# Kernel optimization log

Measured on AMD Instinct MI355X. Metric: run time of the kernel, lower is better.

Reference implementation:

```python
import jax, jax.numpy as jnp
import numpy as np

BS, SL, FD = 8192, 49, 11
D_MODEL, DM2, HEAD = 128, 64, 8
NH, NHID, NLAYER = DM2 // HEAD, 4, 2
ABF = 1.0
XY_IDX = np.array([0, 1, 2, 3, 4, 5, 6, 7, 10])  # x feats + y feat (batch-normed cols)
DEC_IN = D_MODEL + 10  # d_model + len(x_dims + spa_dims)


def tanhshrink(x):
    return x - jnp.tanh(x)


def rope_angles(spa):
    # spa: [bs, sl, 2] -> per-token block angles [bs, sl, 4]
    # block order matches torch.block_diag(Rx(t0), Ry(t0), Rx(t1), Ry(t1))
    thetas = 10000.0 ** ((2.0 - 2.0 * jnp.arange(2, dtype=spa.dtype)) / 8.0)  # d=8, n_thetas=2
    ax = spa[..., 0:1] * thetas  # [bs, sl, 2]
    ay = spa[..., 1:2] * thetas
    return jnp.stack([ax[..., 0], ay[..., 0], ax[..., 1], ay[..., 1]], axis=-1)


def apply_rope(v, ang):
    # v: [bs, nh, s, 8]; ang: [bs, s, 4]. Applies the 8x8 block-diagonal
    # rotation directly on 2-d sub-pairs (same math as R @ v, no 8x8 matmats).
    c = jnp.cos(ang)[:, None]  # [bs, 1, s, 4]
    s = jnp.sin(ang)[:, None]
    v2 = v.reshape(*v.shape[:-1], 4, 2)
    r = jnp.stack([c * v2[..., 0] - s * v2[..., 1],
                   s * v2[..., 0] + c * v2[..., 1]], axis=-1)
    return r.reshape(v.shape)


def heads(x):  # [bs, s, dm2] -> [bs, nh, s, hd]
    b, s, _ = x.shape
    return x.reshape(b, s, NH, HEAD).transpose(0, 2, 1, 3)


def merge(x):  # [bs, nh, s, hd] -> [bs, s, dm2]
    b, h, s, d = x.shape
    return x.transpose(0, 2, 1, 3).reshape(b, s, h * d)


def mlp2(x, w1, b1, w2, b2):
    return tanhshrink(x @ w1 + b1) @ w2 + b2


def forward_impl(input_tensor, dists, bn_gamma, bn_beta,
                 xe_w1, xe_b1, xe_w2, xe_b2, ye_w1, ye_b1, ye_w2, ye_b2,
                 learnable_y, hidden_tokens, Wq, Wk, Wv, Wo, Wq2, Wk2, Wv2, Wo2,
                 dec_w0, dec_b0, dec_w1, dec_b1, dec_w2, dec_b2):
    bs = input_tensor.shape[0]
    # --- NanBatchNorm over x+y feature columns (no NaNs in clean inputs) ---
    xy = input_tensor[:, :, XY_IDX]
    mu = jnp.mean(xy, axis=(0, 1), keepdims=True)
    var = jnp.var(xy, axis=(0, 1), keepdims=True)
    xy = (xy - mu) / jnp.sqrt(var + 1e-5) * bn_gamma + bn_beta
    input_tensor = input_tensor.at[:, :, XY_IDX].set(xy)

    # --- target at last seq position: drop its dist, keep context dists ---
    dists_ctx = dists[:, :-1]                       # [bs, sl-1]
    central_x = input_tensor[:, -1:, :-1]           # [bs, 1, 10] (x + spa feats)

    # --- 2D RoPE angles from spatial coords ---
    ang = rope_angles(input_tensor[:, :, 8:10])     # [bs, sl, 4]

    # --- FCN encoders (two streams a=x, b=y) ---
    x_embed = mlp2(input_tensor[:, :, :8], xe_w1, xe_b1, xe_w2, xe_b2)      # [bs, sl, 64]
    y_embed = mlp2(input_tensor[:, :-1, 10:11], ye_w1, ye_b1, ye_w2, ye_b2)  # [bs, sl-1, 64]
    y_embed = jnp.concatenate([y_embed, jnp.broadcast_to(learnable_y, (bs, 1, DM2))], axis=1)

    ctx = (x_embed[:, :-1], y_embed[:, :-1])
    qry = (x_embed[:, -1:], y_embed[:, -1:])
    ang_ctx, ang_q = ang[:, :-1], ang[:, -1:]
    bias = (-ABF * dists_ctx)[:, None, None, :]     # [bs, 1, 1, sl-1]
    scale = 1.0 / jnp.sqrt(jnp.asarray(HEAD, input_tensor.dtype))

    outs, attn_ws = [], []
    for s in range(2):
        H = jnp.broadcast_to(hidden_tokens, (bs, NHID, DM2))
        for l in range(NLAYER):
            q = heads(H @ Wq[l, s])
            k = apply_rope(heads(ctx[s] @ Wk[l, s]), ang_ctx)
            v = heads(ctx[s] @ Wv[l, s])
            sc = jnp.einsum('bhqd,bhkd->bhqk', q, k) * scale + bias
            a = jax.nn.softmax(sc, axis=-1)
            H = H + merge(jnp.einsum('bhqk,bhkd->bhqd', a, v)) @ Wo[l, s]
        # query cross-attends the inducing tokens
        q = apply_rope(heads(qry[s] @ Wq2[s]), ang_q)
        k = heads(H @ Wk2[s])
        v = heads(H @ Wv2[s])
        sc = jnp.einsum('bhqd,bhkd->bhqk', q, k) * scale
        a = jax.nn.softmax(sc, axis=-1)
        outs.append(merge(jnp.einsum('bhqk,bhkd->bhqd', a, v)) @ Wo2[s])  # [bs, 1, 64]
        attn_ws.append(a)

    encoding = jnp.concatenate(outs, axis=-1)               # [bs, 1, 128]
    encoding = jnp.concatenate([encoding, central_x], axis=-1)  # [bs, 1, 138]
    h = tanhshrink(encoding @ dec_w0 + dec_b0)
    h = tanhshrink(h @ dec_w1 + dec_b1)
    pred = h @ dec_w2 + dec_b2                              # [bs, 1, 1]
    return pred


def setup_inputs() -> dict:
    key = jax.random.key(0)
    ks = jax.random.split(key, 32)
    g = lambda i, shape: 0.05 * jax.random.normal(ks[i], shape, dtype=jnp.float32)
    inp = {
        'input_tensor': jax.random.normal(ks[0], (BS, SL, FD), dtype=jnp.float32),
        'dists': jax.random.uniform(ks[1], (BS, SL), dtype=jnp.float32),
        'target_position': jnp.zeros((3, BS), dtype=jnp.int32),
        'bn_gamma': jnp.ones((9,), jnp.float32),
        'bn_beta': jnp.zeros((9,), jnp.float32),
        'xe_w1': g(2, (8, DM2)), 'xe_b1': jnp.zeros((DM2,), jnp.float32),
        'xe_w2': g(3, (DM2, DM2)), 'xe_b2': jnp.zeros((DM2,), jnp.float32),
        'ye_w1': g(4, (1, DM2)), 'ye_b1': jnp.zeros((DM2,), jnp.float32),
        'ye_w2': g(5, (DM2, DM2)), 'ye_b2': jnp.zeros((DM2,), jnp.float32),
        'learnable_y': g(6, (1, 1, DM2)),
        'hidden_tokens': g(7, (NHID, DM2)),
        'Wq': g(8, (NLAYER, 2, DM2, DM2)), 'Wk': g(9, (NLAYER, 2, DM2, DM2)),
        'Wv': g(10, (NLAYER, 2, DM2, DM2)), 'Wo': g(11, (NLAYER, 2, DM2, DM2)),
        'Wq2': g(12, (2, DM2, DM2)), 'Wk2': g(13, (2, DM2, DM2)),
        'Wv2': g(14, (2, DM2, DM2)), 'Wo2': g(15, (2, DM2, DM2)),
        'dec_w0': g(16, (DEC_IN, 512)), 'dec_b0': jnp.zeros((512,), jnp.float32),
        'dec_w1': g(17, (512, 256)), 'dec_b1': jnp.zeros((256,), jnp.float32),
        'dec_w2': g(18, (256, 1)), 'dec_b2': jnp.zeros((1,), jnp.float32),
    }
    return inp


def reference(input_tensor, dists, target_position, bn_gamma, bn_beta,
              xe_w1, xe_b1, xe_w2, xe_b2, ye_w1, ye_b1, ye_w2, ye_b2,
              learnable_y, hidden_tokens, Wq, Wk, Wv, Wo, Wq2, Wk2, Wv2, Wo2,
              dec_w0, dec_b0, dec_w1, dec_b1, dec_w2, dec_b2):
    # target_position is an index constant (query is the last token by construction)
    return forward_impl(input_tensor, dists, bn_gamma, bn_beta,
                        xe_w1, xe_b1, xe_w2, xe_b2, ye_w1, ye_b1, ye_w2, ye_b2,
                        learnable_y, hidden_tokens, Wq, Wk, Wv, Wo, Wq2, Wk2, Wv2, Wo2,
                        dec_w0, dec_b0, dec_w1, dec_b1, dec_w2, dec_b2)
```

## Files before the change

kernel.cpp:

```cpp
#include <hip/hip_runtime.h>
#include <math.h>

#define BS 8192
#define SL 49
#define FDIM 11
#define ROWS (BS*SL)

__device__ __forceinline__ float tanhshrink_f(float x) {
  float e = __expf(2.f * x);
  return (x - 1.f) + __fdividef(2.f, e + 1.f);
}

__global__ __launch_bounds__(256) void k_stats(const float* __restrict__ inp,
                                               double* __restrict__ gsum) {
  const int nblk = gridDim.x;
  const int per = (ROWS + nblk - 1) / nblk;
  const int r0 = blockIdx.x * per;
  int r1 = r0 + per; if (r1 > ROWS) r1 = ROWS;
  float s[9], q[9];
#pragma unroll
  for (int j = 0; j < 9; ++j) { s[j] = 0.f; q[j] = 0.f; }
  for (int r = r0 + threadIdx.x; r < r1; r += 256) {
    const float* row = inp + r * FDIM;
#pragma unroll
    for (int j = 0; j < 9; ++j) {
      float v = row[j < 8 ? j : 10];
      s[j] += v; q[j] += v * v;
    }
  }
#pragma unroll
  for (int j = 0; j < 9; ++j) {
    for (int off = 32; off; off >>= 1) {
      s[j] += __shfl_down(s[j], off);
      q[j] += __shfl_down(q[j], off);
    }
  }
  __shared__ float red[4][18];
  const int wid = threadIdx.x >> 6;
  const int lane = threadIdx.x & 63;
  if (lane == 0) {
#pragma unroll
    for (int j = 0; j < 9; ++j) { red[wid][j] = s[j]; red[wid][9 + j] = q[j]; }
  }
  __syncthreads();
  if (threadIdx.x < 18) {
    float t = red[0][threadIdx.x] + red[1][threadIdx.x] +
              red[2][threadIdx.x] + red[3][threadIdx.x];
    atomicAdd(&gsum[threadIdx.x], (double)t);
  }
}

__global__ __launch_bounds__(256) void k_finalize(const double* __restrict__ gsum,
                           const float* __restrict__ gamma,
                           const float* __restrict__ beta,
                           const float* __restrict__ hidden,
                           const float* __restrict__ Wq,
                           float* __restrict__ bnp,
                           float* __restrict__ q0g) {
  int tid = threadIdx.x;
  if (tid < 9) {
    const double N = (double)ROWS;
    double mean = gsum[tid] / N;
    double msq  = gsum[9 + tid] / N;
    float var = (float)(msq - mean * mean);
    float sc = gamma[tid] / sqrtf(var + 1e-5f);
    bnp[tid] = sc;
    bnp[9 + tid] = beta[tid] - (float)mean * sc;
  }
  int s = tid >> 7, i2 = (tid >> 6) & 1, c = tid & 63;
  const float* W = Wq + (s << 12);
#pragma unroll
  for (int ii = 0; ii < 2; ++ii) {
    int i = i2 + 2 * ii;
    float a = 0.f;
    for (int k = 0; k < 64; ++k) a += hidden[i * 64 + k] * W[k * 64 + c];
    q0g[s * 256 + i * 64 + c] = a;
  }
}

__global__ __launch_bounds__(256, 4) void k_mega(
    const float* __restrict__ inp, const float* __restrict__ dists,
    const float* __restrict__ bnp, const float* __restrict__ q0g,
    const float* __restrict__ xe_w1, const float* __restrict__ xe_b1,
    const float* __restrict__ xe_w2, const float* __restrict__ xe_b2,
    const float* __restrict__ ye_w1, const float* __restrict__ ye_b1,
    const float* __restrict__ ye_w2, const float* __restrict__ ye_b2,
    const float* __restrict__ learnable_y, const float* __restrict__ hidden_tokens,
    const float* __restrict__ Wq, const float* __restrict__ Wk,
    const float* __restrict__ Wv, const float* __restrict__ Wo,
    const float* __restrict__ Wq2, const float* __restrict__ Wk2,
    const float* __restrict__ Wv2, const float* __restrict__ Wo2,
    float* __restrict__ enc)
{
  __shared__ float raw[49][12];
  __shared__ float cs8[49][8];
  __shared__ float emb[49][64];
  __shared__ float KB[49][68];
  __shared__ float scb[32][52];
  __shared__ float Hs[4][64];
  __shared__ float qb[4][64];
  __shared__ float db[48];
  __shared__ float bnl[18];
  __shared__ float q2[64];
  __shared__ float o1[64];
  __shared__ float a2[32];

  const int tid  = threadIdx.x;
  const int lane = tid & 63;
  const int grp  = tid >> 6;
  const int b    = blockIdx.x >> 1;
  const int s    = blockIdx.x & 1;
  const float scale = 0.35355339059327373f;

  for (int i = tid; i < 49 * FDIM; i += 256) raw[i / FDIM][i % FDIM] = inp[b * (49*FDIM) + i];
  if (tid < 18) bnl[tid] = bnp[tid];
  if (tid >= 64 && tid < 112) db[tid - 64] = dists[b * 49 + (tid - 64)];
  __syncthreads();

  if (tid < 49) {
    float x = raw[tid][8], y = raw[tid][9];
    cs8[tid][0] = cosf(10.f * x); cs8[tid][1] = cosf(10.f * y);
    cs8[tid][2] = cosf(x);        cs8[tid][3] = cosf(y);
    cs8[tid][4] = sinf(10.f * x); cs8[tid][5] = sinf(10.f * y);
    cs8[tid][6] = sinf(x);        cs8[tid][7] = sinf(y);
  }
  for (int i = tid; i < 441; i += 256) {
    int t = i / 9, j = i - t * 9;
    int f = (j < 8) ? j : 10;
    raw[t][f] = raw[t][f] * bnl[j] + bnl[9 + j];
  }
  __syncthreads();

  if (s == 0 && tid < 10) enc[b * 138 + 128 + tid] = raw[48][tid];

  if (s == 0) {
    const float bias1 = xe_b1[lane];
    float acc[13];
#pragma unroll
    for (int j = 0; j < 13; ++j) acc[j] = bias1;
#pragma unroll
    for (int k = 0; k < 8; ++k) {
      float w = xe_w1[k * 64 + lane];
#pragma unroll
      for (int j = 0; j < 13; ++j) {
        int t = grp + 4 * j;
        if (t < 49) acc[j] += raw[t][k] * w;
      }
    }
#pragma unroll
    for (int j = 0; j < 13; ++j) {
      int t = grp + 4 * j;
      if (t < 49) KB[t][lane] = tanhshrink_f(acc[j]);
    }
  } else {
    const float w1y = ye_w1[lane];
    const float b1y = ye_b1[lane];
#pragma unroll
    for (int j = 0; j < 12; ++j) {
      int t = grp + 4 * j;
      KB[t][lane] = tanhshrink_f(raw[t][10] * w1y + b1y);
    }
  }
  __syncthreads();

  if (s == 0) {
    const float b2 = xe_b2[lane];
    float acc[13];
#pragma unroll
    for (int j = 0; j < 13; ++j) acc[j] = b2;
    for (int k = 0; k < 64; k += 4) {
      float w0 = xe_w2[(k + 0) * 64 + lane];
      float w1_ = xe_w2[(k + 1) * 64 + lane];
      float w2_ = xe_w2[(k + 2) * 64 + lane];
      float w3_ = xe_w2[(k + 3) * 64 + lane];
#pragma unroll
      for (int j = 0; j < 13; ++j) {
        int t = grp + 4 * j;
        if (t < 49) {
          float4 cv = *(const float4*)&KB[t][k];
          acc[j] += cv.x * w0 + cv.y * w1_ + cv.z * w2_ + cv.w * w3_;
        }
      }
    }
#pragma unroll
    for (int j = 0; j < 13; ++j) {
      int t = grp + 4 * j;
      if (t < 49) emb[t][lane] = acc[j];
    }
  } else {
    const float b2 = ye_b2[lane];
    float acc[12];
#pragma unroll
    for (int j = 0; j < 12; ++j) acc[j] = b2;
    for (int k = 0; k < 64; k += 4) {
      float w0 = ye_w2[(k + 0) * 64 + lane];
      float w1_ = ye_w2[(k + 1) * 64 + lane];
      float w2_ = ye_w2[(k + 2) * 64 + lane];
      float w3_ = ye_w2[(k + 3) * 64 + lane];
#pragma unroll
      for (int j = 0; j < 12; ++j) {
        float4 cv = *(const float4*)&KB[grp + 4 * j][k];
        acc[j] += cv.x * w0 + cv.y * w1_ + cv.z * w2_ + cv.w * w3_;
      }
    }
#pragma unroll
    for (int j = 0; j < 12; ++j) emb[grp + 4 * j][lane] = acc[j];
    if (tid < 64) emb[48][lane] = learnable_y[lane];
  }
  Hs[grp][lane] = hidden_tokens[grp * 64 + lane];
  __syncthreads();

#pragma unroll 1
  for (int l = 0; l < 2; ++l) {
    const float* Wk_p = Wk + ((l * 2 + s) << 12);
    const float* Wv_p = Wv + ((l * 2 + s) << 12);
    const float* Wo_p = Wo + ((l * 2 + s) << 12);
    if (l == 0) {
      qb[grp][lane] = q0g[s * 256 + tid];
    } else {
      const float* Wq_p = Wq + ((l * 2 + s) << 12);
      float a = 0.f;
      for (int k = 0; k < 64; k += 4) {
        float4 hv = *(const float4*)&Hs[grp][k];
        a += hv.x * Wq_p[(k + 0) * 64 + lane] + hv.y * Wq_p[(k + 1) * 64 + lane]
           + hv.z * Wq_p[(k + 2) * 64 + lane] + hv.w * Wq_p[(k + 3) * 64 + lane];
      }
      qb[grp][lane] = a;
    }
    {
      float aK[12];
#pragma unroll
      for (int j = 0; j < 12; ++j) aK[j] = 0.f;
      for (int k = 0; k < 64; k += 4) {
        float wk0 = Wk_p[(k + 0) * 64 + lane], wk1 = Wk_p[(k + 1) * 64 + lane];
        float wk2 = Wk_p[(k + 2) * 64 + lane], wk3 = Wk_p[(k + 3) * 64 + lane];
#pragma unroll
        for (int j = 0; j < 12; ++j) {
          float4 cv = *(const float4*)&emb[grp + 4 * j][k];
          aK[j] += cv.x * wk0 + cv.y * wk1 + cv.z * wk2 + cv.w * wk3;
        }
      }
      const int p = (lane >> 1) & 3;
      const int odd = lane & 1;
#pragma unroll
      for (int j = 0; j < 12; ++j) {
        int t = grp + 4 * j;
        float other = __shfl_xor(aK[j], 1);
        float co = cs8[t][p], si = cs8[t][4 + p];
        KB[t][lane] = odd ? (si * other + co * aK[j]) : (co * aK[j] - si * other);
      }
    }
    __syncthreads();
    {
      const int t0 = tid & 7;
      const int i  = (tid >> 3) & 3;
      const int h  = tid >> 5;
      const int r  = tid >> 3;
      float4 qa = *(const float4*)&qb[i][h * 8];
      float4 qc = *(const float4*)&qb[i][h * 8 + 4];
      float v[6];
#pragma unroll
      for (int j = 0; j < 6; ++j) {
        int t = t0 + 8 * j;
        float4 ka = *(const float4*)&KB[t][h * 8];
        float4 kc = *(const float4*)&KB[t][h * 8 + 4];
        float a = qa.x * ka.x + qa.y * ka.y + qa.z * ka.z + qa.w * ka.w
                + qc.x * kc.x + qc.y * kc.y + qc.z * kc.z + qc.w * kc.w;
        v[j] = a * scale - db[t];
      }
      float m = fmaxf(fmaxf(fmaxf(v[0], v[1]), fmaxf(v[2], v[3])), fmaxf(v[4], v[5]));
      m = fmaxf(m, __shfl_xor(m, 1));
      m = fmaxf(m, __shfl_xor(m, 2));
      m = fmaxf(m, __shfl_xor(m, 4));
      float sum = 0.f;
#pragma unroll
      for (int j = 0; j < 6; ++j) { v[j] = __expf(v[j] - m); sum += v[j]; }
      sum += __shfl_xor(sum, 1);
      sum += __shfl_xor(sum, 2);
      sum += __shfl_xor(sum, 4);
      float inv = 1.f / sum;
#pragma unroll
      for (int j = 0; j < 6; ++j) scb[r][t0 + 8 * j] = v[j] * inv;
    }
    __syncthreads();
    {
      float acc[8];
#pragma unroll
      for (int m = 0; m < 8; ++m) acc[m] = 0.f;
      for (int tt = 0; tt < 48; tt += 4) {
        float e0 = emb[tt + 0][lane], e1 = emb[tt + 1][lane];
        float e2 = emb[tt + 2][lane], e3 = emb[tt + 3][lane];
#pragma unroll
        for (int m = 0; m < 8; ++m) {
          float4 sc4 = *(const float4*)&scb[grp + 4 * m][tt];
          acc[m] += sc4.x * e0 + sc4.y * e1 + sc4.z * e2 + sc4.w * e3;
        }
      }
#pragma unroll
      for (int m = 0; m < 8; ++m) KB[grp + 4 * m][lane] = acc[m];
    }
    __syncthreads();
    {
      const int r = ((lane >> 3) << 2) + grp;
      float a = 0.f;
      for (int c = 0; c < 64; c += 4) {
        float4 tv = *(const float4*)&KB[r][c];
        a += tv.x * Wv_p[(c + 0) * 64 + lane] + tv.y * Wv_p[(c + 1) * 64 + lane]
           + tv.z * Wv_p[(c + 2) * 64 + lane] + tv.w * Wv_p[(c + 3) * 64 + lane];
      }
      qb[grp][lane] = a;
    }
    __syncthreads();
    {
      float a = Hs[grp][lane];
      for (int k = 0; k < 64; k += 4) {
        float4 av = *(const float4*)&qb[grp][k];
        a += av.x * Wo_p[(k + 0) * 64 + lane] + av.y * Wo_p[(k + 1) * 64 + lane]
           + av.z * Wo_p[(k + 2) * 64 + lane] + av.w * Wo_p[(k + 3) * 64 + lane];
      }
      Hs[grp][lane] = a;
    }
    __syncthreads();
  }

  const float* Wq2_p = Wq2 + (s << 12);
  const float* Wk2_p = Wk2 + (s << 12);
  const float* Wv2_p = Wv2 + (s << 12);
  const float* Wo2_p = Wo2 + (s << 12);
  if (tid < 64) {
    float a = 0.f;
    for (int k = 0; k < 64; k += 4) {
      float4 cv = *(const float4*)&emb[48][k];
      a += cv.x * Wq2_p[(k + 0) * 64 + lane] + cv.y * Wq2_p[(k + 1) * 64 + lane]
         + cv.z * Wq2_p[(k + 2) * 64 + lane] + cv.w * Wq2_p[(k + 3) * 64 + lane];
    }
    float other = __shfl_xor(a, 1);
    int p = (lane >> 1) & 3;
    float co = cs8[48][p], si = cs8[48][4 + p];
    q2[lane] = (lane & 1) ? (si * other + co * a) : (co * a - si * other);
  }
  {
    float aK = 0.f, aV = 0.f;
    for (int k = 0; k < 64; k += 4) {
      float4 hv = *(const float4*)&Hs[grp][k];
      aK += hv.x * Wk2_p[(k + 0) * 64 + lane] + hv.y * Wk2_p[(k + 1) * 64 + lane]
          + hv.z * Wk2_p[(k + 2) * 64 + lane] + hv.w * Wk2_p[(k + 3) * 64 + lane];
      aV += hv.x * Wv2_p[(k + 0) * 64 + lane] + hv.y * Wv2_p[(k + 1) * 64 + lane]
          + hv.z * Wv2_p[(k + 2) * 64 + lane] + hv.w * Wv2_p[(k + 3) * 64 + lane];
    }
    KB[grp][lane] = aK;
    KB[8 + grp][lane] = aV;
  }
  __syncthreads();
  if (tid < 32) {
    int h = tid >> 2, i = tid & 3;
    float a = 0.f;
#pragma unroll
    for (int d = 0; d < 8; ++d) a += q2[h * 8 + d] * KB[i][h * 8 + d];
    a *= scale;
    float m = fmaxf(a, __shfl_xor(a, 1));
    m = fmaxf(m, __shfl_xor(m, 2));
    float e = __expf(a - m);
    float sum = e + __shfl_xor(e, 1);
    sum += __shfl_xor(sum, 2);
    a2[tid] = e / sum;
  }
  __syncthreads();
  if (tid < 64) {
    int h = lane >> 3;
    float a = 0.f;
#pragma unroll
    for (int i = 0; i < 4; ++i) a += a2[h * 4 + i] * KB[8 + i][lane];
    o1[lane] = a;
  }
  __syncthreads();
  if (tid < 64) {
    float a = 0.f;
    for (int k = 0; k < 64; k += 4) {
      float4 ov = *(const float4*)&o1[k];
      a += ov.x * Wo2_p[(k + 0) * 64 + lane] + ov.y * Wo2_p[(k + 1) * 64 + lane]
         + ov.z * Wo2_p[(k + 2) * 64 + lane] + ov.w * Wo2_p[(k + 3) * 64 + lane];
    }
    enc[b * 138 + s * 64 + lane] = a;
  }
}

__global__ __launch_bounds__(256) void k_dec(
    const float* __restrict__ enc,
    const float* __restrict__ w0, const float* __restrict__ b0,
    const float* __restrict__ w1, const float* __restrict__ b1,
    const float* __restrict__ w2, const float* __restrict__ b2,
    float* __restrict__ out)
{
  __shared__ float encs[16][140];
  __shared__ float h0s[16][512];
  __shared__ float h1s[16][256];
  const int tid = threadIdx.x;
  const int rb = blockIdx.x * 16;

  for (int i = tid; i < 16 * 138; i += 256) {
    int r = i / 138, k = i - r * 138;
    encs[r][k] = enc[(rb + r) * 138 + k];
  }
  __syncthreads();
  {
    float acc0[16], acc1[16];
    const float bb0 = b0[tid], bb1 = b0[tid + 256];
#pragma unroll
    for (int r = 0; r < 16; ++r) { acc0[r] = bb0; acc1[r] = bb1; }
    for (int k = 0; k < 136; k += 4) {
      float wa0 = w0[(k + 0) * 512 + tid], wa1 = w0[(k + 1) * 512 + tid];
      float wa2 = w0[(k + 2) * 512 + tid], wa3 = w0[(k + 3) * 512 + tid];
      float wb0 = w0[(k + 0) * 512 + tid + 256], wb1 = w0[(k + 1) * 512 + tid + 256];
      float wb2 = w0[(k + 2) * 512 + tid + 256], wb3 = w0[(k + 3) * 512 + tid + 256];
#pragma unroll
      for (int r = 0; r < 16; ++r) {
        float4 ev = *(const float4*)&encs[r][k];
        acc0[r] += ev.x * wa0 + ev.y * wa1 + ev.z * wa2 + ev.w * wa3;
        acc1[r] += ev.x * wb0 + ev.y * wb1 + ev.z * wb2 + ev.w * wb3;
      }
    }
    for (int k = 136; k < 138; ++k) {
      float wa = w0[k * 512 + tid], wb = w0[k * 512 + tid + 256];
#pragma unroll
      for (int r = 0; r < 16; ++r) {
        float e = encs[r][k];
        acc0[r] += e * wa; acc1[r] += e * wb;
      }
    }
#pragma unroll
    for (int r = 0; r < 16; ++r) {
      float a = acc0[r]; h0s[r][tid] = a - tanhf(a);
      a = acc1[r];       h0s[r][tid + 256] = a - tanhf(a);
    }
  }
  __syncthreads();
  {
    float acc[16];
    const float bb = b1[tid];
#pragma unroll
    for (int r = 0; r < 16; ++r) acc[r] = bb;
    for (int k = 0; k < 512; k += 4) {
      float ww0 = w1[(k + 0) * 256 + tid], ww1 = w1[(k + 1) * 256 + tid];
      float ww2 = w1[(k + 2) * 256 + tid], ww3 = w1[(k + 3) * 256 + tid];
#pragma unroll
      for (int r = 0; r < 16; ++r) {
        float4 hv = *(const float4*)&h0s[r][k];
        acc[r] += hv.x * ww0 + hv.y * ww1 + hv.z * ww2 + hv.w * ww3;
      }
    }
#pragma unroll
    for (int r = 0; r < 16; ++r) { float a = acc[r]; h1s[r][tid] = a - tanhf(a); }
  }
  __syncthreads();
  {
    int r = tid >> 4, l16 = tid & 15;
    float a = 0.f;
    for (int kk = 0; kk < 16; ++kk) {
      int k = l16 + 16 * kk;
      a += h1s[r][k] * w2[k];
    }
    for (int off = 8; off; off >>= 1) a += __shfl_down(a, off, 16);
    if (l16 == 0) out[rb + r] = a + b2[0];
  }
}

extern "C" void kernel_launch(void* const* d_in, const int* in_sizes, int n_in,
                              void* d_out, int out_size, void* d_ws, size_t ws_size,
                              hipStream_t stream) {
  const float* inp        = (const float*)d_in[0];
  const float* dists      = (const float*)d_in[1];
  const float* bn_gamma   = (const float*)d_in[3];
  const float* bn_beta    = (const float*)d_in[4];
  const float* xe_w1      = (const float*)d_in[5];
  const float* xe_b1      = (const float*)d_in[6];
  const float* xe_w2      = (const float*)d_in[7];
  const float* xe_b2      = (const float*)d_in[8];
  const float* ye_w1      = (const float*)d_in[9];
  const float* ye_b1      = (const float*)d_in[10];
  const float* ye_w2      = (const float*)d_in[11];
  const float* ye_b2      = (const float*)d_in[12];
  const float* learnable  = (const float*)d_in[13];
  const float* hidden     = (const float*)d_in[14];
  const float* Wq         = (const float*)d_in[15];
  const float* Wk         = (const float*)d_in[16];
  const float* Wv         = (const float*)d_in[17];
  const float* Wo         = (const float*)d_in[18];
  const float* Wq2        = (const float*)d_in[19];
  const float* Wk2        = (const float*)d_in[20];
  const float* Wv2        = (const float*)d_in[21];
  const float* Wo2        = (const float*)d_in[22];
  const float* dec_w0     = (const float*)d_in[23];
  const float* dec_b0     = (const float*)d_in[24];
  const float* dec_w1     = (const float*)d_in[25];
  const float* dec_b1     = (const float*)d_in[26];
  const float* dec_w2     = (const float*)d_in[27];
  const float* dec_b2     = (const float*)d_in[28];

  double* gsum = (double*)d_ws;
  float*  bnp  = (float*)((char*)d_ws + 256);
  float*  q0g  = (float*)((char*)d_ws + 512);
  float*  enc  = (float*)((char*)d_ws + 2560);

  hipMemsetAsync(d_ws, 0, 256, stream);
  k_stats   <<<512, 256, 0, stream>>>(inp, gsum);
  k_finalize<<<1, 256, 0, stream>>>(gsum, bn_gamma, bn_beta, hidden, Wq, bnp, q0g);
  k_mega    <<<BS * 2, 256, 0, stream>>>(inp, dists, bnp, q0g,
                                         xe_w1, xe_b1, xe_w2, xe_b2,
                                         ye_w1, ye_b1, ye_w2, ye_b2,
                                         learnable, hidden,
                                         Wq, Wk, Wv, Wo, Wq2, Wk2, Wv2, Wo2, enc);
  k_dec     <<<BS / 16, 256, 0, stream>>>(enc, dec_w0, dec_b0, dec_w1, dec_b1,
                                          dec_w2, dec_b2, (float*)d_out);
}
```

Baseline: 1.007 ms.

## Alias shared memory and split score buffer to raise occupancy of encoder and decoder

The encoder kernel packs its shared buffers into one aliased array and halves the attention score buffer, processing the 32 score rows in two passes with extra barriers. It peels token 48 out of the embedding loops to remove predicated iterations, and raises the launch-bounds occupancy target from 4 to 5. The decoder kernel processes 8 rows per block instead of 16, uses the fast tanhshrink, and reduces over 32 lanes. This trades extra synchronisation and weight reloads per row for smaller shared-memory and register footprints, aiming at more resident blocks.

```diff
diff --git a/kernel.cpp b/kernel.cpp
--- a/kernel.cpp
+++ b/kernel.cpp
@@ -78,7 +78,7 @@
   }
 }
 
-__global__ __launch_bounds__(256, 4) void k_mega(
+__global__ __launch_bounds__(256, 5) void k_mega(
     const float* __restrict__ inp, const float* __restrict__ dists,
     const float* __restrict__ bnp, const float* __restrict__ q0g,
     const float* __restrict__ xe_w1, const float* __restrict__ xe_b1,
@@ -92,18 +92,20 @@
     const float* __restrict__ Wv2, const float* __restrict__ Wo2,
     float* __restrict__ enc)
 {
-  __shared__ float raw[49][12];
-  __shared__ float cs8[49][8];
-  __shared__ float emb[49][64];
-  __shared__ float KB[49][68];
-  __shared__ float scb[32][52];
-  __shared__ float Hs[4][64];
-  __shared__ float qb[4][64];
-  __shared__ float db[48];
-  __shared__ float bnl[18];
-  __shared__ float q2[64];
-  __shared__ float o1[64];
-  __shared__ float a2[32];
+  __shared__ float smem[8120];
+  float (*raw)[12]  = (float(*)[12])(smem);
+  float*  bnl       = smem + 588;
+  float*  h1r48     = smem + 608;
+  float (*scb)[48]  = (float(*)[48])(smem);
+  float*  q2        = smem;
+  float*  o1        = smem + 64;
+  float*  a2        = smem + 128;
+  float (*cs8)[8]   = (float(*)[8])(smem + 768);
+  float (*emb)[64]  = (float(*)[64])(smem + 1160);
+  float (*KB)[68]   = (float(*)[68])(smem + 4296);
+  float (*qb)[64]   = (float(*)[64])(smem + 7560);
+  float (*Hs)[64]   = (float(*)[64])(smem + 7816);
+  float*  db        = smem + 8072;
 
   const int tid  = threadIdx.x;
   const int lane = tid & 63;
@@ -135,23 +137,19 @@
 
   if (s == 0) {
     const float bias1 = xe_b1[lane];
-    float acc[13];
-#pragma unroll
-    for (int j = 0; j < 13; ++j) acc[j] = bias1;
+    float acc[12], a48 = bias1;
+#pragma unroll
+    for (int j = 0; j < 12; ++j) acc[j] = bias1;
 #pragma unroll
     for (int k = 0; k < 8; ++k) {
       float w = xe_w1[k * 64 + lane];
 #pragma unroll
-      for (int j = 0; j < 13; ++j) {
-        int t = grp + 4 * j;
-        if (t < 49) acc[j] += raw[t][k] * w;
-      }
-    }
-#pragma unroll
-    for (int j = 0; j < 13; ++j) {
-      int t = grp + 4 * j;
-      if (t < 49) KB[t][lane] = tanhshrink_f(acc[j]);
-    }
+      for (int j = 0; j < 12; ++j) acc[j] += raw[grp + 4 * j][k] * w;
+      a48 += raw[48][k] * w;
+    }
+#pragma unroll
+    for (int j = 0; j < 12; ++j) KB[grp + 4 * j][lane] = tanhshrink_f(acc[j]);
+    if (grp == 0) h1r48[lane] = tanhshrink_f(a48);
   } else {
     const float w1y = ye_w1[lane];
     const float b1y = ye_b1[lane];
@@ -165,28 +163,25 @@
 
   if (s == 0) {
     const float b2 = xe_b2[lane];
-    float acc[13];
-#pragma unroll
-    for (int j = 0; j < 13; ++j) acc[j] = b2;
+    float acc[12], a48 = b2;
+#pragma unroll
+    for (int j = 0; j < 12; ++j) acc[j] = b2;
     for (int k = 0; k < 64; k += 4) {
       float w0 = xe_w2[(k + 0) * 64 + lane];
       float w1_ = xe_w2[(k + 1) * 64 + lane];
       float w2_ = xe_w2[(k + 2) * 64 + lane];
       float w3_ = xe_w2[(k + 3) * 64 + lane];
 #pragma unroll
-      for (int j = 0; j < 13; ++j) {
-        int t = grp + 4 * j;
-        if (t < 49) {
-          float4 cv = *(const float4*)&KB[t][k];
-          acc[j] += cv.x * w0 + cv.y * w1_ + cv.z * w2_ + cv.w * w3_;
-        }
-      }
-    }
-#pragma unroll
-    for (int j = 0; j < 13; ++j) {
-      int t = grp + 4 * j;
-      if (t < 49) emb[t][lane] = acc[j];
-    }
+      for (int j = 0; j < 12; ++j) {
+        float4 cv = *(const float4*)&KB[grp + 4 * j][k];
+        acc[j] += cv.x * w0 + cv.y * w1_ + cv.z * w2_ + cv.w * w3_;
+      }
+      float4 c48 = *(const float4*)&h1r48[k];
+      a48 += c48.x * w0 + c48.y * w1_ + c48.z * w2_ + c48.w * w3_;
+    }
+#pragma unroll
+    for (int j = 0; j < 12; ++j) emb[grp + 4 * j][lane] = acc[j];
+    if (grp == 0) emb[48][lane] = a48;
   } else {
     const float b2 = ye_b2[lane];
     float acc[12];
@@ -280,26 +275,53 @@
       sum += __shfl_xor(sum, 4);
       float inv = 1.f / sum;
 #pragma unroll
-      for (int j = 0; j < 6; ++j) scb[r][t0 + 8 * j] = v[j] * inv;
-    }
-    __syncthreads();
-    {
-      float acc[8];
-#pragma unroll
-      for (int m = 0; m < 8; ++m) acc[m] = 0.f;
-      for (int tt = 0; tt < 48; tt += 4) {
-        float e0 = emb[tt + 0][lane], e1 = emb[tt + 1][lane];
-        float e2 = emb[tt + 2][lane], e3 = emb[tt + 3][lane];
-#pragma unroll
-        for (int m = 0; m < 8; ++m) {
-          float4 sc4 = *(const float4*)&scb[grp + 4 * m][tt];
-          acc[m] += sc4.x * e0 + sc4.y * e1 + sc4.z * e2 + sc4.w * e3;
+      for (int j = 0; j < 6; ++j) v[j] *= inv;
+
+      if (r < 16) {
+#pragma unroll
+        for (int j = 0; j < 6; ++j) scb[r][t0 + 8 * j] = v[j];
+      }
+      __syncthreads();
+      {
+        float accT[4];
+#pragma unroll
+        for (int m2 = 0; m2 < 4; ++m2) accT[m2] = 0.f;
+        for (int tt = 0; tt < 48; tt += 4) {
+          float e0 = emb[tt + 0][lane], e1 = emb[tt + 1][lane];
+          float e2 = emb[tt + 2][lane], e3 = emb[tt + 3][lane];
+#pragma unroll
+          for (int m2 = 0; m2 < 4; ++m2) {
+            float4 s4 = *(const float4*)&scb[grp + 4 * m2][tt];
+            accT[m2] += s4.x * e0 + s4.y * e1 + s4.z * e2 + s4.w * e3;
+          }
         }
-      }
-#pragma unroll
-      for (int m = 0; m < 8; ++m) KB[grp + 4 * m][lane] = acc[m];
-    }
-    __syncthreads();
+#pragma unroll
+        for (int m2 = 0; m2 < 4; ++m2) KB[grp + 4 * m2][lane] = accT[m2];
+      }
+      __syncthreads();
+      if (r >= 16) {
+#pragma unroll
+        for (int j = 0; j < 6; ++j) scb[r - 16][t0 + 8 * j] = v[j];
+      }
+      __syncthreads();
+      {
+        float accT[4];
+#pragma unroll
+        for (int m2 = 0; m2 < 4; ++m2) accT[m2] = 0.f;
+        for (int tt = 0; tt < 48; tt += 4) {
+          float e0 = emb[tt + 0][lane], e1 = emb[tt + 1][lane];
+          float e2 = emb[tt + 2][lane], e3 = emb[tt + 3][lane];
+#pragma unroll
+          for (int m2 = 0; m2 < 4; ++m2) {
+            float4 s4 = *(const float4*)&scb[grp + 4 * m2][tt];
+            accT[m2] += s4.x * e0 + s4.y * e1 + s4.z * e2 + s4.w * e3;
+          }
+        }
+#pragma unroll
+        for (int m2 = 0; m2 < 4; ++m2) KB[16 + grp + 4 * m2][lane] = accT[m2];
+      }
+      __syncthreads();
+    }
     {
       const int r = ((lane >> 3) << 2) + grp;
       float a = 0.f;
@@ -385,36 +407,36 @@
   }
 }
 
-__global__ __launch_bounds__(256) void k_dec(
+__global__ __launch_bounds__(256, 5) void k_dec(
     const float* __restrict__ enc,
     const float* __restrict__ w0, const float* __restrict__ b0,
     const float* __restrict__ w1, const float* __restrict__ b1,
     const float* __restrict__ w2, const float* __restrict__ b2,
     float* __restrict__ out)
 {
-  __shared__ float encs[16][140];
-  __shared__ float h0s[16][512];
-  __shared__ float h1s[16][256];
+  __shared__ float encs[8][140];
+  __shared__ float h0s[8][512];
+  __shared__ float h1s[8][256];
   const int tid = threadIdx.x;
-  const int rb = blockIdx.x * 16;
-
-  for (int i = tid; i < 16 * 138; i += 256) {
+  const int rb = blockIdx.x * 8;
+
+  for (int i = tid; i < 8 * 138; i += 256) {
     int r = i / 138, k = i - r * 138;
     encs[r][k] = enc[(rb + r) * 138 + k];
   }
   __syncthreads();
   {
-    float acc0[16], acc1[16];
+    float acc0[8], acc1[8];
     const float bb0 = b0[tid], bb1 = b0[tid + 256];
 #pragma unroll
-    for (int r = 0; r < 16; ++r) { acc0[r] = bb0; acc1[r] = bb1; }
+    for (int r = 0; r < 8; ++r) { acc0[r] = bb0; acc1[r] = bb1; }
     for (int k = 0; k < 136; k += 4) {
       float wa0 = w0[(k + 0) * 512 + tid], wa1 = w0[(k + 1) * 512 + tid];
       float wa2 = w0[(k + 2) * 512 + tid], wa3 = w0[(k + 3) * 512 + tid];
       float wb0 = w0[(k + 0) * 512 + tid + 256], wb1 = w0[(k + 1) * 512 + tid + 256];
       float wb2 = w0[(k + 2) * 512 + tid + 256], wb3 = w0[(k + 3) * 512 + tid + 256];
 #pragma unroll
-      for (int r = 0; r < 16; ++r) {
+      for (int r = 0; r < 8; ++r) {
         float4 ev = *(const float4*)&encs[r][k];
         acc0[r] += ev.x * wa0 + ev.y * wa1 + ev.z * wa2 + ev.w * wa3;
         acc1[r] += ev.x * wb0 + ev.y * wb1 + ev.z * wb2 + ev.w * wb3;
@@ -423,45 +445,46 @@
     for (int k = 136; k < 138; ++k) {
       float wa = w0[k * 512 + tid], wb = w0[k * 512 + tid + 256];
 #pragma unroll
-      for (int r = 0; r < 16; ++r) {
+      for (int r = 0; r < 8; ++r) {
         float e = encs[r][k];
         acc0[r] += e * wa; acc1[r] += e * wb;
       }
     }
 #pragma unroll
-    for (int r = 0; r < 16; ++r) {
-      float a = acc0[r]; h0s[r][tid] = a - tanhf(a);
-      a = acc1[r];       h0s[r][tid + 256] = a - tanhf(a);
+    for (int r = 0; r < 8; ++r) {
+      h0s[r][tid] = tanhshrink_f(acc0[r]);
+      h0s[r][tid + 256] = tanhshrink_f(acc1[r]);
     }
   }
   __syncthreads();
   {
-    float acc[16];
+    float acc[8];
     const float bb = b1[tid];
 #pragma unroll
-    for (int r = 0; r < 16; ++r) acc[r] = bb;
+    for (int r = 0; r < 8; ++r) acc[r] = bb;
     for (int k = 0; k < 512; k += 4) {
       float ww0 = w1[(k + 0) * 256 + tid], ww1 = w1[(k + 1) * 256 + tid];
       float ww2 = w1[(k + 2) * 256 + tid], ww3 = w1[(k + 3) * 256 + tid];
 #pragma unroll
-      for (int r = 0; r < 16; ++r) {
+      for (int r = 0; r < 8; ++r) {
         float4 hv = *(const float4*)&h0s[r][k];
         acc[r] += hv.x * ww0 + hv.y * ww1 + hv.z * ww2 + hv.w * ww3;
       }
     }
 #pragma unroll
-    for (int r = 0; r < 16; ++r) { float a = acc[r]; h1s[r][tid] = a - tanhf(a); }
+    for (int r = 0; r < 8; ++r) h1s[r][tid] = tanhshrink_f(acc[r]);
   }
   __syncthreads();
   {
-    int r = tid >> 4, l16 = tid & 15;
+    int r = tid >> 5, l32 = tid & 31;
     float a = 0.f;
-    for (int kk = 0; kk < 16; ++kk) {
-      int k = l16 + 16 * kk;
+#pragma unroll
+    for (int kk = 0; kk < 8; ++kk) {
+      int k = l32 + 32 * kk;
       a += h1s[r][k] * w2[k];
     }
-    for (int off = 8; off; off >>= 1) a += __shfl_down(a, off, 16);
-    if (l16 == 0) out[rb + r] = a + b2[0];
+    for (int off = 16; off; off >>= 1) a += __shfl_down(a, off, 32);
+    if (l32 == 0) out[rb + r] = a + b2[0];
   }
 }
 
@@ -510,6 +533,6 @@
                                          ye_w1, ye_b1, ye_w2, ye_b2,
                                          learnable, hidden,
                                          Wq, Wk, Wv, Wo, Wq2, Wk2, Wv2, Wo2, enc);
-  k_dec     <<<BS / 16, 256, 0, stream>>>(enc, dec_w0, dec_b0, dec_w1, dec_b1,
-                                          dec_w2, dec_b2, (float*)d_out);
+  k_dec     <<<BS / 8, 256, 0, stream>>>(enc, dec_w0, dec_b0, dec_w1, dec_b1,
+                                         dec_w2, dec_b2, (float*)d_out);
 }
```

Measured after the change: 1.174 ms. 16.6% more time.
